# Kernel tuning notes

Hardware: AMD Instinct MI355X
Metric: run time of the kernel (lower is better)

## Reference

```python
import jax, jax.numpy as jnp
import numpy as np
from jax.scipy.special import logsumexp

N_NODES = 20000
N_FEAT = 64
N_TPL = 10
TPL_NODES = 10
K_NEIGH = 15  # local neighborhood cap -> local graph size kloc = K+1 (self first)
N_EDGES = N_NODES * 16


def setup_inputs() -> dict:
    key = jax.random.key(0)
    k1, k2, k3, k4, k5 = jax.random.split(key, 5)
    x = jax.random.normal(k1, (N_NODES, N_FEAT), dtype=jnp.float32)
    edge_index = jax.random.randint(k2, (2, N_EDGES), 0, N_NODES, dtype=jnp.int32)
    # template_initialisation: randint{0,1} adjacency + N(0, 0.01) noise
    adj = jax.random.randint(k3, (N_TPL, TPL_NODES, TPL_NODES), 0, 2).astype(jnp.float32)
    templates = adj + 0.01 * jax.random.normal(k4, (N_TPL, TPL_NODES, TPL_NODES), dtype=jnp.float32)
    # template features ~ N(0.0012, 0.02)
    templates_features = 0.0012 + 0.02 * jax.random.normal(
        k5, (N_TPL, TPL_NODES, N_FEAT), dtype=jnp.float32)
    alpha0 = jnp.array([0.5], dtype=jnp.float32)
    return {"x": x, "edge_index": edge_index, "templates": templates,
            "templates_features": templates_features, "alpha0": alpha0}


def _fgw_distances(x, edge_index, templates, templates_features, alpha0,
                   K=K_NEIGH, n_outer=3, n_sink=5):
    """Per-node fused GW distance between the node's local (star) subgraph and
    each learned template, solved with an entropic proximal / Sinkhorn scheme.
    Returns [N, T]."""
    N, F = x.shape
    Tn, n, _ = templates.shape
    kloc = K + 1

    # ---- build fixed-size neighbor lists from edge_index (int ops, constant) ----
    src, dst = edge_index[0], edge_index[1]
    E = src.shape[0]
    order = jnp.argsort(src)
    src_s, dst_s = src[order], dst[order]
    deg = jnp.zeros((N,), jnp.int32).at[src].add(1)
    start = jnp.cumsum(deg) - deg                       # CSR row starts
    rank = jnp.arange(E, dtype=jnp.int32) - start[src_s]  # position within each node's list
    # rank >= K falls out of bounds -> dropped
    neigh = jnp.zeros((N, K), jnp.int32).at[src_s, rank].set(dst_s, mode="drop")
    nb_mask = (jnp.arange(K)[None, :] < jnp.minimum(deg, K)[:, None]).astype(x.dtype)  # [N,K]

    # ---- local graphs: self node first, then up to K neighbors ----
    xloc = jnp.concatenate([x[:, None, :], x[neigh]], axis=1)  # [N, kloc, F]
    m = jnp.concatenate([jnp.ones((N, 1), x.dtype), nb_mask], axis=1)  # [N, kloc]
    p = m / jnp.sum(m, -1, keepdims=True)                # node-side marginal
    q = jnp.full((n,), 1.0 / n, x.dtype)                 # template-side marginal

    # star adjacency of the 1-hop neighborhood
    row0 = jnp.concatenate([jnp.zeros((N, 1), x.dtype), nb_mask], axis=1)
    C1 = jnp.zeros((N, kloc, kloc), x.dtype).at[:, 0, :].set(row0).at[:, :, 0].set(row0)
    C2 = templates  # [T, n, n]

    # feature cost M[n_node, t, k, m] = ||xloc - y||^2
    M = (jnp.sum(xloc ** 2, -1)[:, None, :, None]
         + jnp.sum(templates_features ** 2, -1)[None, :, None, :]
         - 2.0 * jnp.einsum("nkf,tmf->ntkm", xloc, templates_features))

    alpha = jax.nn.sigmoid(alpha0)[0]

    # GW square-loss constant terms (Peyre et al. trick)
    hC1 = jnp.einsum("nkl,nl->nk", C1 ** 2, p)   # [N, kloc]
    hC2 = jnp.einsum("tmr,r->tm", C2 ** 2, q)    # [T, n]
    constC = hC1[:, None, :, None] + hC2[None, :, None, :]

    def gw_tens(Tp):  # Tp: [N, T, kloc, n]
        tmp = jnp.einsum("nkl,ntlm->ntkm", C1, Tp)
        return constC - 2.0 * jnp.einsum("ntkm,trm->ntkr", tmp, C2)

    eps = 0.05 * jax.lax.stop_gradient(jnp.mean(M)) + 1e-6
    logp = jnp.where(m > 0, jnp.log(jnp.maximum(p, 1e-30)), -1e9)[:, None, :]  # [N,1,kloc]
    logq = jnp.log(q)  # [n]

    Tp = p[:, None, :, None] * q[None, None, None, :]  # independent-coupling init
    f = jnp.zeros((N, Tn, kloc), x.dtype)
    g = jnp.zeros((N, Tn, n), x.dtype)
    for _ in range(n_outer):  # outer FGW linearization steps
        G = (1.0 - alpha) * M + 2.0 * alpha * gw_tens(Tp)
        logK = -G / eps
        for _ in range(n_sink):  # log-domain Sinkhorn on linearized cost
            f = eps * (logp - logsumexp(logK + g[:, :, None, :] / eps, axis=-1))
            g = eps * (logq - logsumexp(logK + f[:, :, :, None] / eps, axis=-2))
        Tp = jnp.exp(logK + f[:, :, :, None] / eps + g[:, :, None, :] / eps)

    dist = ((1.0 - alpha) * jnp.sum(M * Tp, axis=(-2, -1))
            + alpha * jnp.sum(gw_tens(Tp) * Tp, axis=(-2, -1)))
    return dist  # [N, T]


def reference(x, edge_index, templates, templates_features, alpha0):
    return _fgw_distances(x, edge_index, templates, templates_features, alpha0)
```

## Files before the change

### kernel.cpp

```cpp
#include <hip/hip_runtime.h>

#define N_NODES 20000
#define NPAIRS  10000
#define N_EDGES 320000
#define CAP     64
#define KN      15

typedef _Float16 half_t;
typedef _Float16 half2_t __attribute__((ext_vector_type(2)));

#define P_ALPHA 0
#define P_BETA  1
#define P_IEPS2 2
#define P_EPS   3
#define P_HC2   16
#define P_RSC2  216
#define P_F1    316

#define OFF_CNT    0u
#define OFF_COUNTS 80000u
#define OFF_STATS  160000u
#define OFF_FLAG   160520u
#define OFF_NBC    160528u
#define OFF_NEIGH  240528u
#define OFF_XH     1440528u
#define OFF_S2X    4000528u
#define OFF_BUF    1440528u
#define OFF_PARAMS 6560528u

#define TF_STRIDE 648

template<int CTRL>
__device__ __forceinline__ float dpp_add(float v) {
  int s = __builtin_bit_cast(int, v);
  int r = __builtin_amdgcn_update_dpp(0, s, CTRL, 0xF, 0xF, true);
  return v + __builtin_bit_cast(float, r);
}
__device__ __forceinline__ float sum16(float v) {
  v = dpp_add<0x128>(v);
  v = dpp_add<0x124>(v);
  v = dpp_add<0x122>(v);
  v = dpp_add<0x121>(v);
  return v;
}
__device__ __forceinline__ float bcast16(float v) {
  return __builtin_bit_cast(float,
      __builtin_amdgcn_ds_swizzle(__builtin_bit_cast(int, v), 0x010));
}
__device__ __forceinline__ float fdot2(half2_t a, half2_t b, float c) {
  return __builtin_amdgcn_fdot2(a, b, c, false);
}

__global__ void k_scatter(const int* __restrict__ ei, int* __restrict__ cnt,
                          int* __restrict__ buf) {
  int e = blockIdx.x * blockDim.x + threadIdx.x;
  if (e >= N_EDGES) return;
  int s = ei[e];
  int slot = atomicAdd(&cnt[s], 1);
  if (slot < CAP) buf[s * CAP + slot] = e;
}

__global__ void k_select(const int* __restrict__ ei, const int* __restrict__ cnt,
                         const int* __restrict__ buf, int* __restrict__ nbc_g,
                         int* __restrict__ neigh, int* __restrict__ counts) {
  int w = (blockIdx.x * blockDim.x + threadIdx.x) >> 6;
  int lane = threadIdx.x & 63;
  if (w >= N_NODES) return;
  const int* dst = ei + N_EDGES;
  int c = cnt[w];
  int cc = c < CAP ? c : CAP;
  int e = (lane < cc) ? buf[w * CAP + lane] : 0x7fffffff;
  int nb = c < KN ? c : KN;
  bool sel;
  if (cc <= KN) {
    sel = lane < cc;
  } else {
    int rank = 0;
    for (int j = 0; j < cc; j++) {
      int ej = __shfl(e, j);
      rank += (ej < e) ? 1 : 0;
    }
    sel = (e != 0x7fffffff) && (rank < KN);
  }
  unsigned long long mask = __ballot(sel);
  if (sel) {
    int pos = __popcll(mask & ((1ull << lane) - 1ull));
    int d = dst[e];
    neigh[w * KN + pos] = d;
    atomicAdd(&counts[d], 1);
  }
  if (lane == 0) {
    nbc_g[w] = nb;
    atomicAdd(&counts[w], 1);
    if (nb < KN) atomicAdd(&counts[0], KN - nb);
  }
}

#define STATS_BLOCKS 512
__global__ void k_stats(const float* __restrict__ x, const int* __restrict__ counts,
                        double* __restrict__ stats, int* __restrict__ flag,
                        half_t* __restrict__ xh, float* __restrict__ s2xh,
                        const float* __restrict__ tf, const float* __restrict__ c2,
                        const float* __restrict__ alpha0, float* __restrict__ params) {
  int lane = threadIdx.x & 63;
  int wid = threadIdx.x >> 6;
  int gw = blockIdx.x * 4 + wid;
  float accx = 0.f, acc2 = 0.f;
  for (int u = gw; u < N_NODES; u += STATS_BLOCKS * 4) {
    float w = (float)counts[u];
    float val = x[u * 64 + lane];
    half_t h = (half_t)val;
    xh[u * 64 + lane] = h;
    float hv = (float)h;
    float sq = hv * hv;
#pragma unroll
    for (int off = 32; off > 0; off >>= 1) sq += __shfl_xor(sq, off, 64);
    if (lane == 0) s2xh[u] = sq;
    accx += w * val;
    acc2 += w * val * val;
  }
#pragma unroll
  for (int off = 32; off > 0; off >>= 1) acc2 += __shfl_xor(acc2, off, 64);
  __shared__ float redx[4][64];
  __shared__ float red2[4];
  __shared__ int lastsh;
  redx[wid][lane] = accx;
  if (lane == 0) red2[wid] = acc2;
  __syncthreads();
  if (threadIdx.x < 64) {
    float s = redx[0][threadIdx.x] + redx[1][threadIdx.x] +
              redx[2][threadIdx.x] + redx[3][threadIdx.x];
    atomicAdd(&stats[1 + threadIdx.x], (double)s);
  }
  if (threadIdx.x == 0)
    atomicAdd(&stats[0], (double)(red2[0] + red2[1] + red2[2] + red2[3]));
  __syncthreads();
  if (threadIdx.x == 0) {
    __threadfence();
    int old = atomicAdd(flag, 1);
    lastsh = (old == STATS_BLOCKS - 1) ? 1 : 0;
  }
  __syncthreads();
  if (!lastsh) return;
  __threadfence();
  __shared__ float sh[4];
  int tid = threadIdx.x;
  if (tid < 64) {
    float s = 0.f, s2 = 0.f;
    for (int tm = 0; tm < 100; tm++) { float v = tf[tm * 64 + tid]; s += v; s2 += v * v; }
    double inv16N = 1.0 / (double)(N_NODES * 16);
    double cross = (stats[1 + tid] * inv16N) * ((double)s / 100.0);
    double B = (double)s2 / 100.0;
    double term = B - 2.0 * cross;
#pragma unroll
    for (int off = 32; off > 0; off >>= 1) term += __shfl_xor(term, off, 64);
    if (tid == 0) {
      double A = stats[0] * inv16N;
      double meanM = A + term;
      float eps = (float)(0.05 * meanM) + 1e-6f;
      float a0 = alpha0[0];
      float alpha = 1.f / (1.f + expf(-a0));
      params[P_ALPHA] = alpha;
      params[P_BETA]  = 1.f - alpha;
      params[P_IEPS2] = 1.4426950408889634f / eps;
      params[P_EPS]   = eps;
      sh[0] = alpha; sh[1] = 1.f - alpha; sh[2] = 1.4426950408889634f / eps;
    }
  }
  __syncthreads();
  if (tid < 100) {
    float alpha = sh[0], beta = sh[1], ieps2 = sh[2];
    int t = tid / 10, mm = tid % 10;
    float h = 0.f;
    for (int r = 0; r < 10; r++) { float cv = c2[t * 100 + mm * 10 + r]; h += cv * cv; }
    float hc2v = 0.1f * h;
    params[P_HC2 + tid] = hc2v;
    float s2 = 0.f;
    for (int f = 0; f < 64; f++) { float v = tf[tid * 64 + f]; s2 += v * v; }
    float rs = 0.f;
    for (int m2 = 0; m2 < 10; m2++) rs += c2[t * 100 + mm * 10 + m2];
    params[P_RSC2 + tid] = rs;
    params[P_F1 + tid] = (beta * s2 + 2.0f * alpha * hc2v) * (-ieps2);
  }
}

__global__ void __launch_bounds__(320, 6)
k_main(const half_t* __restrict__ xh, const float* __restrict__ tf_g,
       const float* __restrict__ c2_g, const int* __restrict__ nbc_g,
       const int* __restrict__ neigh_g, const float* __restrict__ params,
       const float* __restrict__ s2x_g, float* __restrict__ out) {
  __shared__ __align__(16) half_t tf_l[10 * TF_STRIDE];
  __shared__ __align__(16) float c2_l[1000];
  __shared__ __align__(16) float hc2_l[100];
  __shared__ __align__(16) float rsc2_l[100];
  __shared__ __align__(16) float F1_l[100];
  __shared__ __align__(16) float bsb_l[20][10][2];

  const int tid = threadIdx.x;
  const int node_s = tid / 160;
  const int s = tid % 160;
  const int t = s >> 4;
  const int k = s & 15;
  const bool k0 = (k == 0);
  const int grp = node_s * 10 + t;

  for (int i = tid; i < 6400; i += 320) {
    int tt = i / 640, rem = i - tt * 640;
    tf_l[tt * TF_STRIDE + rem] = (half_t)tf_g[i];
  }
  for (int i = tid; i < 1000; i += 320) c2_l[i] = c2_g[i];
  if (tid < 100) {
    hc2_l[tid]  = params[P_HC2 + tid];
    rsc2_l[tid] = params[P_RSC2 + tid];
    F1_l[tid]   = params[P_F1 + tid];
  }

  const float alpha = params[P_ALPHA];
  const float beta  = params[P_BETA];
  const float ieps2 = params[P_IEPS2];
  const float eps   = params[P_EPS];
  const float niep  = -ieps2;
  const float twoal = 2.0f * alpha;
  const float ctv10 = 0.2f * twoal * ieps2;
  const float cab   = 2.0f * beta * ieps2;
  const float c_a2d = -eps * 0.69314718056f;
  const float twoal01 = 0.1f * twoal;

  const int idx_c2 = t * 100 + ((k < 10) ? k : 9) * 10;
  __syncthreads();

  const int kk = (k == 0) ? 0 : (k - 1);
  int p = blockIdx.x;
  int nb_pf = nbc_g[2 * p + node_s];
  int nbr_pf = neigh_g[(2 * p + node_s) * KN + kk];

#pragma unroll 1
  for (; p < NPAIRS; p += gridDim.x) {
    const int v = 2 * p + node_s;
    const int nb = nb_pf;
    const int srcn = (k == 0) ? v : (kk < nb ? nbr_pf : 0);
    const float s2x = s2x_g[srcn];
    const uint4* xr = (const uint4*)(xh + (size_t)srcn * 64);

    {
      int vn = 2 * (p + gridDim.x) + node_s;
      vn = vn < N_NODES ? vn : 0;
      nb_pf = nbc_g[vn];
      nbr_pf = neigh_g[vn * KN + kk];
    }

    float acc[10];
#pragma unroll
    for (int m = 0; m < 10; m++) acc[m] = 0.0f;
    {
      const half_t* tfb = &tf_l[t * TF_STRIDE];
#pragma unroll 1
      for (int ch = 0; ch < 2; ch++) {
        uint4 xq[4];
#pragma unroll
        for (int c = 0; c < 4; c++) xq[c] = xr[ch * 4 + c];
#pragma unroll
        for (int c = 0; c < 4; c++) {
          half2_t x0 = __builtin_bit_cast(half2_t, xq[c].x);
          half2_t x1 = __builtin_bit_cast(half2_t, xq[c].y);
          half2_t x2 = __builtin_bit_cast(half2_t, xq[c].z);
          half2_t x3 = __builtin_bit_cast(half2_t, xq[c].w);
#pragma unroll
          for (int m = 0; m < 10; m++) {
            uint4 tq = *(const uint4*)&tfb[m * 64 + (ch * 4 + c) * 8];
            float a = acc[m];
            a = fdot2(__builtin_bit_cast(half2_t, tq.x), x0, a);
            a = fdot2(__builtin_bit_cast(half2_t, tq.y), x1, a);
            a = fdot2(__builtin_bit_cast(half2_t, tq.z), x2, a);
            a = fdot2(__builtin_bit_cast(half2_t, tq.w), x3, a);
            acc[m] = a;
          }
        }
      }
    }

    const float inv = 1.0f / (float)(1 + nb);
    const float pk = (k <= nb) ? inv : 0.0f;
    const float hC1k = (k == 0) ? (float)nb * inv : ((k <= nb) ? inv : 0.0f);
    const float base = (beta * s2x + twoal * hC1k) * niep;
    const float ctm  = ctv10 * ((k == 0) ? (float)nb * inv : inv);

    float Ab[10];
#pragma unroll
    for (int j = 0; j < 5; j++) {
      float2 f1 = *(const float2*)&F1_l[t * 10 + 2 * j];
      Ab[2 * j]     = fmaf(cab, acc[2 * j],     f1.x + base);
      Ab[2 * j + 1] = fmaf(cab, acc[2 * j + 1], f1.y + base);
    }

    float K[10], vv[10];
    float u = 1.0f;
#pragma unroll
    for (int m = 0; m < 10; m++) vv[m] = 1.0f;

#pragma unroll
    for (int j = 0; j < 5; j++) {
      float2 rs = *(const float2*)&rsc2_l[t * 10 + 2 * j];
      K[2 * j]     = __builtin_amdgcn_exp2f(fmaf(ctm, rs.x, Ab[2 * j]));
      K[2 * j + 1] = __builtin_amdgcn_exp2f(fmaf(ctm, rs.y, Ab[2 * j + 1]));
    }

#pragma unroll 1
    for (int o = 0; o < 3; o++) {
#pragma unroll 1
      for (int it = 0; it < 5; it++) {
        float kv = 0.0f;
#pragma unroll
        for (int m = 0; m < 10; m++) kv = fmaf(K[m], vv[m], kv);
        u = pk * __builtin_amdgcn_rcpf(kv);
#pragma unroll
        for (int m = 0; m < 10; m++) {
          float w = sum16(K[m] * u);
          vv[m] = __builtin_amdgcn_rcpf(w);
        }
      }
      if (o == 2) break;
      {
        float B = 0.0f, SB = 0.0f;
#pragma unroll
        for (int j = 0; j < 5; j++) {
          float2 c2p = *(const float2*)&c2_l[idx_c2 + 2 * j];
          float tka = K[2 * j] * vv[2 * j] * u;
          float tkb = K[2 * j + 1] * vv[2 * j + 1] * u;
          B  = fmaf(bcast16(tka), c2p.x, B);
          SB = fmaf(sum16(tka),   c2p.x, SB);
          B  = fmaf(bcast16(tkb), c2p.y, B);
          SB = fmaf(sum16(tkb),   c2p.y, SB);
        }
        if (k < 10) { bsb_l[grp][k][0] = B; bsb_l[grp][k][1] = SB; }
        __threadfence_block();
#pragma unroll
        for (int j = 0; j < 5; j++) {
          float4 bv = *(const float4*)&bsb_l[grp][2 * j][0];
          float tva = k0 ? (bv.y - bv.x) : bv.x;
          float tvb = k0 ? (bv.w - bv.z) : bv.z;
          K[2 * j]     = __builtin_amdgcn_exp2f(fmaf(ctv10, tva, Ab[2 * j]));
          K[2 * j + 1] = __builtin_amdgcn_exp2f(fmaf(ctv10, tvb, Ab[2 * j + 1]));
        }
        __threadfence_block();
      }
    }

    {
      float tk[10];
      float B = 0.0f, SB = 0.0f;
#pragma unroll
      for (int j = 0; j < 5; j++) {
        float2 c2p = *(const float2*)&c2_l[idx_c2 + 2 * j];
        tk[2 * j]     = K[2 * j] * vv[2 * j] * u;
        tk[2 * j + 1] = K[2 * j + 1] * vv[2 * j + 1] * u;
        B  = fmaf(bcast16(tk[2 * j]), c2p.x, B);
        SB = fmaf(sum16(tk[2 * j]),   c2p.x, SB);
        B  = fmaf(bcast16(tk[2 * j + 1]), c2p.y, B);
        SB = fmaf(sum16(tk[2 * j + 1]),   c2p.y, SB);
      }
      if (k < 10) { bsb_l[grp][k][0] = B; bsb_l[grp][k][1] = SB; }
      __threadfence_block();
      float dd = 0.0f;
#pragma unroll
      for (int j = 0; j < 5; j++) {
        float4 bv = *(const float4*)&bsb_l[grp][2 * j][0];
        float2 h2 = *(const float2*)&hc2_l[t * 10 + 2 * j];
        float tva = k0 ? (bv.y - bv.x) : bv.x;
        float tvb = k0 ? (bv.w - bv.z) : bv.z;
        float c1a = fmaf(alpha, hC1k + h2.x, twoal01 * tva);
        float c1b = fmaf(alpha, hC1k + h2.y, twoal01 * tvb);
        float coa = fmaf(c_a2d, Ab[2 * j], -c1a);
        float cob = fmaf(c_a2d, Ab[2 * j + 1], -c1b);
        dd = fmaf(coa, tk[2 * j], dd);
        dd = fmaf(cob, tk[2 * j + 1], dd);
      }
      __threadfence_block();
      dd = sum16(dd * 0.1f);
      if (k == 0) out[v * 10 + t] = dd;
    }
  }
}

extern "C" void kernel_launch(void* const* d_in, const int* in_sizes, int n_in,
                              void* d_out, int out_size, void* d_ws, size_t ws_size,
                              hipStream_t stream) {
  const float* x  = (const float*)d_in[0];
  const int*   ei = (const int*)d_in[1];
  const float* c2 = (const float*)d_in[2];
  const float* tf = (const float*)d_in[3];
  const float* a0 = (const float*)d_in[4];
  float* out = (float*)d_out;
  char* ws = (char*)d_ws;
  int*    cnt    = (int*)(ws + OFF_CNT);
  int*    counts = (int*)(ws + OFF_COUNTS);
  double* stats  = (double*)(ws + OFF_STATS);
  int*    flag   = (int*)(ws + OFF_FLAG);
  int*    nbc    = (int*)(ws + OFF_NBC);
  int*    neigh  = (int*)(ws + OFF_NEIGH);
  int*    buf    = (int*)(ws + OFF_BUF);
  half_t* xh     = (half_t*)(ws + OFF_XH);
  float*  s2xh   = (float*)(ws + OFF_S2X);
  float*  params = (float*)(ws + OFF_PARAMS);
  (void)in_sizes; (void)n_in; (void)out_size; (void)ws_size;

  hipMemsetAsync(ws, 0, 160528, stream);
  k_scatter<<<N_EDGES / 256, 256, 0, stream>>>(ei, cnt, buf);
  k_select<<<(N_NODES * 64 + 255) / 256, 256, 0, stream>>>(ei, cnt, buf, nbc, neigh, counts);
  k_stats<<<STATS_BLOCKS, 256, 0, stream>>>(x, counts, stats, flag, xh, s2xh,
                                            tf, c2, a0, params);
  k_main<<<2500, 320, 0, stream>>>(xh, tf, c2, nbc, neigh, params, s2xh, out);
}
```

Baseline: 444.6 us.

## Fuse scatter, select and stats kernels into one persistent kernel with grid barriers

Merges the three preprocessing kernels into a single persistent kernel of 512 blocks, separated by software grid barriers built on atomic counters in the workspace. This removes two kernel launches and their inter-kernel gaps. It also lowers the k_main launch-bounds occupancy hint from 6 to 4 and splits the Sinkhorn kv dot product into two accumulators to shorten the FMA dependency chain. The grid barrier relies on all 512 blocks being co-resident, which risks deadlock if they are not. The select and scatter phases now run with far fewer threads in grid-stride loops.

```diff
diff --git a/kernel.cpp b/kernel.cpp
--- a/kernel.cpp
+++ b/kernel.cpp
@@ -21,14 +21,18 @@
 #define OFF_COUNTS 80000u
 #define OFF_STATS  160000u
 #define OFF_FLAG   160520u
-#define OFF_NBC    160528u
-#define OFF_NEIGH  240528u
-#define OFF_XH     1440528u
-#define OFF_S2X    4000528u
-#define OFF_BUF    1440528u
-#define OFF_PARAMS 6560528u
+#define OFF_BAR1   160524u
+#define OFF_BAR2   160528u
+#define OFF_NBC    160544u
+#define OFF_NEIGH  240544u
+#define OFF_XH     1440544u
+#define OFF_S2X    4000544u
+#define OFF_BUF    1440544u
+#define OFF_PARAMS 6560544u
+#define MEMSET_LEN 160544u
 
 #define TF_STRIDE 648
+#define PREP_BLOCKS 512
 
 template<int CTRL>
 __device__ __forceinline__ float dpp_add(float v) {
@@ -51,140 +55,159 @@
   return __builtin_amdgcn_fdot2(a, b, c, false);
 }
 
-__global__ void k_scatter(const int* __restrict__ ei, int* __restrict__ cnt,
-                          int* __restrict__ buf) {
-  int e = blockIdx.x * blockDim.x + threadIdx.x;
-  if (e >= N_EDGES) return;
-  int s = ei[e];
-  int slot = atomicAdd(&cnt[s], 1);
-  if (slot < CAP) buf[s * CAP + slot] = e;
-}
-
-__global__ void k_select(const int* __restrict__ ei, const int* __restrict__ cnt,
-                         const int* __restrict__ buf, int* __restrict__ nbc_g,
-                         int* __restrict__ neigh, int* __restrict__ counts) {
-  int w = (blockIdx.x * blockDim.x + threadIdx.x) >> 6;
-  int lane = threadIdx.x & 63;
-  if (w >= N_NODES) return;
-  const int* dst = ei + N_EDGES;
-  int c = cnt[w];
-  int cc = c < CAP ? c : CAP;
-  int e = (lane < cc) ? buf[w * CAP + lane] : 0x7fffffff;
-  int nb = c < KN ? c : KN;
-  bool sel;
-  if (cc <= KN) {
-    sel = lane < cc;
-  } else {
-    int rank = 0;
-    for (int j = 0; j < cc; j++) {
-      int ej = __shfl(e, j);
-      rank += (ej < e) ? 1 : 0;
-    }
-    sel = (e != 0x7fffffff) && (rank < KN);
-  }
-  unsigned long long mask = __ballot(sel);
-  if (sel) {
-    int pos = __popcll(mask & ((1ull << lane) - 1ull));
-    int d = dst[e];
-    neigh[w * KN + pos] = d;
-    atomicAdd(&counts[d], 1);
-  }
-  if (lane == 0) {
-    nbc_g[w] = nb;
-    atomicAdd(&counts[w], 1);
-    if (nb < KN) atomicAdd(&counts[0], KN - nb);
-  }
-}
-
-#define STATS_BLOCKS 512
-__global__ void k_stats(const float* __restrict__ x, const int* __restrict__ counts,
-                        double* __restrict__ stats, int* __restrict__ flag,
-                        half_t* __restrict__ xh, float* __restrict__ s2xh,
-                        const float* __restrict__ tf, const float* __restrict__ c2,
-                        const float* __restrict__ alpha0, float* __restrict__ params) {
-  int lane = threadIdx.x & 63;
-  int wid = threadIdx.x >> 6;
-  int gw = blockIdx.x * 4 + wid;
-  float accx = 0.f, acc2 = 0.f;
-  for (int u = gw; u < N_NODES; u += STATS_BLOCKS * 4) {
-    float w = (float)counts[u];
-    float val = x[u * 64 + lane];
-    half_t h = (half_t)val;
-    xh[u * 64 + lane] = h;
-    float hv = (float)h;
-    float sq = hv * hv;
-#pragma unroll
-    for (int off = 32; off > 0; off >>= 1) sq += __shfl_xor(sq, off, 64);
-    if (lane == 0) s2xh[u] = sq;
-    accx += w * val;
-    acc2 += w * val * val;
-  }
-#pragma unroll
-  for (int off = 32; off > 0; off >>= 1) acc2 += __shfl_xor(acc2, off, 64);
-  __shared__ float redx[4][64];
-  __shared__ float red2[4];
-  __shared__ int lastsh;
-  redx[wid][lane] = accx;
-  if (lane == 0) red2[wid] = acc2;
+__device__ __forceinline__ void gridbar(int* ctr) {
   __syncthreads();
-  if (threadIdx.x < 64) {
-    float s = redx[0][threadIdx.x] + redx[1][threadIdx.x] +
-              redx[2][threadIdx.x] + redx[3][threadIdx.x];
-    atomicAdd(&stats[1 + threadIdx.x], (double)s);
-  }
-  if (threadIdx.x == 0)
-    atomicAdd(&stats[0], (double)(red2[0] + red2[1] + red2[2] + red2[3]));
+  __threadfence();
+  if (threadIdx.x == 0) {
+    int arrived = __hip_atomic_fetch_add(ctr, 1, __ATOMIC_ACQ_REL,
+                                         __HIP_MEMORY_SCOPE_AGENT) + 1;
+    if (arrived == PREP_BLOCKS) {
+      __hip_atomic_fetch_add(ctr, 1, __ATOMIC_ACQ_REL, __HIP_MEMORY_SCOPE_AGENT);
+    } else {
+      while (__hip_atomic_load(ctr, __ATOMIC_ACQUIRE,
+                               __HIP_MEMORY_SCOPE_AGENT) <= PREP_BLOCKS)
+        __builtin_amdgcn_s_sleep(1);
+    }
+  }
   __syncthreads();
-  if (threadIdx.x == 0) {
+  __threadfence();
+}
+
+__global__ void __launch_bounds__(256)
+k_prep(const int* __restrict__ ei, const float* __restrict__ x,
+       int* cnt, int* buf, int* nbc_g, int* neigh, int* counts,
+       double* stats, int* flag, int* bar1, int* bar2,
+       half_t* xh, float* s2xh,
+       const float* __restrict__ tf, const float* __restrict__ c2,
+       const float* __restrict__ alpha0, float* params) {
+  const int tid = threadIdx.x;
+  const int gtid = blockIdx.x * 256 + tid;
+  const int lane = tid & 63;
+  const int wid = tid >> 6;
+
+  for (int e = gtid; e < N_EDGES; e += PREP_BLOCKS * 256) {
+    int s = ei[e];
+    int slot = atomicAdd(&cnt[s], 1);
+    if (slot < CAP) buf[s * CAP + slot] = e;
+  }
+  gridbar(bar1);
+
+  {
+    const int* dst = ei + N_EDGES;
+    const int gwave = blockIdx.x * 4 + wid;
+    for (int w = gwave; w < N_NODES; w += PREP_BLOCKS * 4) {
+      int c = cnt[w];
+      int cc = c < CAP ? c : CAP;
+      int e = (lane < cc) ? buf[w * CAP + lane] : 0x7fffffff;
+      int nb = c < KN ? c : KN;
+      bool sel;
+      if (cc <= KN) {
+        sel = lane < cc;
+      } else {
+        int rank = 0;
+        for (int j = 0; j < cc; j++) {
+          int ej = __shfl(e, j);
+          rank += (ej < e) ? 1 : 0;
+        }
+        sel = (e != 0x7fffffff) && (rank < KN);
+      }
+      unsigned long long mask = __ballot(sel);
+      if (sel) {
+        int pos = __popcll(mask & ((1ull << lane) - 1ull));
+        int d = dst[e];
+        neigh[w * KN + pos] = d;
+        atomicAdd(&counts[d], 1);
+      }
+      if (lane == 0) {
+        nbc_g[w] = nb;
+        atomicAdd(&counts[w], 1);
+        if (nb < KN) atomicAdd(&counts[0], KN - nb);
+      }
+    }
+  }
+  gridbar(bar2);
+
+  {
+    const int gw = blockIdx.x * 4 + wid;
+    float accx = 0.f, acc2 = 0.f;
+    for (int u = gw; u < N_NODES; u += PREP_BLOCKS * 4) {
+      float w = (float)counts[u];
+      float val = x[u * 64 + lane];
+      half_t h = (half_t)val;
+      xh[u * 64 + lane] = h;
+      float hv = (float)h;
+      float sq = hv * hv;
+#pragma unroll
+      for (int off = 32; off > 0; off >>= 1) sq += __shfl_xor(sq, off, 64);
+      if (lane == 0) s2xh[u] = sq;
+      accx += w * val;
+      acc2 += w * val * val;
+    }
+#pragma unroll
+    for (int off = 32; off > 0; off >>= 1) acc2 += __shfl_xor(acc2, off, 64);
+    __shared__ float redx[4][64];
+    __shared__ float red2[4];
+    __shared__ int lastsh;
+    redx[wid][lane] = accx;
+    if (lane == 0) red2[wid] = acc2;
+    __syncthreads();
+    if (tid < 64) {
+      float s = redx[0][tid] + redx[1][tid] + redx[2][tid] + redx[3][tid];
+      atomicAdd(&stats[1 + tid], (double)s);
+    }
+    if (tid == 0)
+      atomicAdd(&stats[0], (double)(red2[0] + red2[1] + red2[2] + red2[3]));
+    __syncthreads();
+    if (tid == 0) {
+      __threadfence();
+      int old = atomicAdd(flag, 1);
+      lastsh = (old == PREP_BLOCKS - 1) ? 1 : 0;
+    }
+    __syncthreads();
+    if (!lastsh) return;
     __threadfence();
-    int old = atomicAdd(flag, 1);
-    lastsh = (old == STATS_BLOCKS - 1) ? 1 : 0;
-  }
-  __syncthreads();
-  if (!lastsh) return;
-  __threadfence();
-  __shared__ float sh[4];
-  int tid = threadIdx.x;
-  if (tid < 64) {
-    float s = 0.f, s2 = 0.f;
-    for (int tm = 0; tm < 100; tm++) { float v = tf[tm * 64 + tid]; s += v; s2 += v * v; }
-    double inv16N = 1.0 / (double)(N_NODES * 16);
-    double cross = (stats[1 + tid] * inv16N) * ((double)s / 100.0);
-    double B = (double)s2 / 100.0;
-    double term = B - 2.0 * cross;
-#pragma unroll
-    for (int off = 32; off > 0; off >>= 1) term += __shfl_xor(term, off, 64);
-    if (tid == 0) {
-      double A = stats[0] * inv16N;
-      double meanM = A + term;
-      float eps = (float)(0.05 * meanM) + 1e-6f;
-      float a0 = alpha0[0];
-      float alpha = 1.f / (1.f + expf(-a0));
-      params[P_ALPHA] = alpha;
-      params[P_BETA]  = 1.f - alpha;
-      params[P_IEPS2] = 1.4426950408889634f / eps;
-      params[P_EPS]   = eps;
-      sh[0] = alpha; sh[1] = 1.f - alpha; sh[2] = 1.4426950408889634f / eps;
-    }
-  }
-  __syncthreads();
-  if (tid < 100) {
-    float alpha = sh[0], beta = sh[1], ieps2 = sh[2];
-    int t = tid / 10, mm = tid % 10;
-    float h = 0.f;
-    for (int r = 0; r < 10; r++) { float cv = c2[t * 100 + mm * 10 + r]; h += cv * cv; }
-    float hc2v = 0.1f * h;
-    params[P_HC2 + tid] = hc2v;
-    float s2 = 0.f;
-    for (int f = 0; f < 64; f++) { float v = tf[tid * 64 + f]; s2 += v * v; }
-    float rs = 0.f;
-    for (int m2 = 0; m2 < 10; m2++) rs += c2[t * 100 + mm * 10 + m2];
-    params[P_RSC2 + tid] = rs;
-    params[P_F1 + tid] = (beta * s2 + 2.0f * alpha * hc2v) * (-ieps2);
-  }
-}
-
-__global__ void __launch_bounds__(320, 6)
+    __shared__ float sh[4];
+    if (tid < 64) {
+      float s = 0.f, s2 = 0.f;
+      for (int tm = 0; tm < 100; tm++) { float v = tf[tm * 64 + tid]; s += v; s2 += v * v; }
+      double inv16N = 1.0 / (double)(N_NODES * 16);
+      double cross = (stats[1 + tid] * inv16N) * ((double)s / 100.0);
+      double B = (double)s2 / 100.0;
+      double term = B - 2.0 * cross;
+#pragma unroll
+      for (int off = 32; off > 0; off >>= 1) term += __shfl_xor(term, off, 64);
+      if (tid == 0) {
+        double A = stats[0] * inv16N;
+        double meanM = A + term;
+        float eps = (float)(0.05 * meanM) + 1e-6f;
+        float a0 = alpha0[0];
+        float alpha = 1.f / (1.f + expf(-a0));
+        params[P_ALPHA] = alpha;
+        params[P_BETA]  = 1.f - alpha;
+        params[P_IEPS2] = 1.4426950408889634f / eps;
+        params[P_EPS]   = eps;
+        sh[0] = alpha; sh[1] = 1.f - alpha; sh[2] = 1.4426950408889634f / eps;
+      }
+    }
+    __syncthreads();
+    if (tid < 100) {
+      float alpha = sh[0], beta = sh[1], ieps2 = sh[2];
+      int t = tid / 10, mm = tid % 10;
+      float h = 0.f;
+      for (int r = 0; r < 10; r++) { float cv = c2[t * 100 + mm * 10 + r]; h += cv * cv; }
+      float hc2v = 0.1f * h;
+      params[P_HC2 + tid] = hc2v;
+      float s2 = 0.f;
+      for (int f = 0; f < 64; f++) { float v = tf[tid * 64 + f]; s2 += v * v; }
+      float rs = 0.f;
+      for (int m2 = 0; m2 < 10; m2++) rs += c2[t * 100 + mm * 10 + m2];
+      params[P_RSC2 + tid] = rs;
+      params[P_F1 + tid] = (beta * s2 + 2.0f * alpha * hc2v) * (-ieps2);
+    }
+  }
+}
+
+__global__ void __launch_bounds__(320, 4)
 k_main(const half_t* __restrict__ xh, const float* __restrict__ tf_g,
        const float* __restrict__ c2_g, const int* __restrict__ nbc_g,
        const int* __restrict__ neigh_g, const float* __restrict__ params,
@@ -309,10 +332,13 @@
     for (int o = 0; o < 3; o++) {
 #pragma unroll 1
       for (int it = 0; it < 5; it++) {
-        float kv = 0.0f;
-#pragma unroll
-        for (int m = 0; m < 10; m++) kv = fmaf(K[m], vv[m], kv);
-        u = pk * __builtin_amdgcn_rcpf(kv);
+        float kv0 = 0.0f, kv1 = 0.0f;
+#pragma unroll
+        for (int m = 0; m < 10; m += 2) {
+          kv0 = fmaf(K[m],     vv[m],     kv0);
+          kv1 = fmaf(K[m + 1], vv[m + 1], kv1);
+        }
+        u = pk * __builtin_amdgcn_rcpf(kv0 + kv1);
 #pragma unroll
         for (int m = 0; m < 10; m++) {
           float w = sum16(K[m] * u);
@@ -396,6 +422,8 @@
   int*    counts = (int*)(ws + OFF_COUNTS);
   double* stats  = (double*)(ws + OFF_STATS);
   int*    flag   = (int*)(ws + OFF_FLAG);
+  int*    bar1   = (int*)(ws + OFF_BAR1);
+  int*    bar2   = (int*)(ws + OFF_BAR2);
   int*    nbc    = (int*)(ws + OFF_NBC);
   int*    neigh  = (int*)(ws + OFF_NEIGH);
   int*    buf    = (int*)(ws + OFF_BUF);
@@ -404,10 +432,9 @@
   float*  params = (float*)(ws + OFF_PARAMS);
   (void)in_sizes; (void)n_in; (void)out_size; (void)ws_size;
 
-  hipMemsetAsync(ws, 0, 160528, stream);
-  k_scatter<<<N_EDGES / 256, 256, 0, stream>>>(ei, cnt, buf);
-  k_select<<<(N_NODES * 64 + 255) / 256, 256, 0, stream>>>(ei, cnt, buf, nbc, neigh, counts);
-  k_stats<<<STATS_BLOCKS, 256, 0, stream>>>(x, counts, stats, flag, xh, s2xh,
-                                            tf, c2, a0, params);
+  hipMemsetAsync(ws, 0, MEMSET_LEN, stream);
+  k_prep<<<PREP_BLOCKS, 256, 0, stream>>>(ei, x, cnt, buf, nbc, neigh, counts,
+                                          stats, flag, bar1, bar2, xh, s2xh,
+                                          tf, c2, a0, params);
   k_main<<<2500, 320, 0, stream>>>(xh, tf, c2, nbc, neigh, params, s2xh, out);
 }
```

New measurement: 710.6 us. 59.8% more time.
